# Optimization experiments

Hardware: AMD Instinct MI355X
Metric: run time of the kernel (lower is better)

The kernel has to match this reference:

```python
import jax, jax.numpy as jnp
import numpy as np

D = 8192          # dimension (high_dim_mode since > 1000)
M = 1_600_000     # ~0.05 * D*(D-1) pairs after the i>j mask
RIEMANN_SHIFT = 0.5


def _lower_tri_pairs(rng, d, m):
    # Sample m unique strictly-lower-triangular (i, j) positions (i > j).
    total = d * (d - 1) // 2
    k = rng.choice(total, size=m, replace=False)
    kf = k.astype(np.float64)
    i = np.floor((1.0 + np.sqrt(1.0 + 8.0 * kf)) / 2.0).astype(np.int64)
    # fix possible off-by-one from float sqrt
    tri = i * (i - 1) // 2
    i = np.where(tri > k, i - 1, i)
    tri = i * (i - 1) // 2
    j = k - tri
    return i, j


def setup_inputs() -> dict:
    key = jax.random.key(0)
    k1, k2 = jax.random.split(key)
    rng = np.random.default_rng(0)

    i, j = _lower_tri_pairs(rng, D, M)
    interaction_indices = jnp.asarray(np.stack([i, j]))  # [2, M] int64

    local_scale = 1.0 / D ** 0.75
    h_local = jax.random.normal(k1, (D,), dtype=jnp.float32) * local_scale + RIEMANN_SHIFT

    dim_factor = 1.0 / (D ** 0.9 * np.log(D))
    V_interaction = jax.random.normal(k2, (M,), dtype=jnp.float32) * dim_factor

    return {
        "h_local": h_local,
        "V_interaction": V_interaction,
        "interaction_indices": interaction_indices,
        "dimension": D,
    }


def reference(h_local, V_interaction, interaction_indices, dimension) -> jnp.ndarray:
    d = h_local.shape[0]
    # scatter interaction values into strict lower triangle (set semantics,
    # indices are unique so set == torch assignment)
    H_int = jnp.zeros((d, d), dtype=h_local.dtype)
    H_int = H_int.at[interaction_indices[0], interaction_indices[1]].set(V_interaction)
    H_int = H_int + H_int.T  # symmetrize
    interaction_scale = 1.0 - 0.2 / np.sqrt(np.log(dimension))
    return jnp.diag(h_local) + H_int * interaction_scale
```

## Files before the change

kernel.cpp:

```cpp
#include <hip/hip_runtime.h>
#include <math.h>


#define NCHUNK   512
#define NBKT     2048
#define BCAP     8
#define NROW     8192
#define OVB      512
#define OVCAP    64
#define SENTK    0xFFFFFFFFu
#define GCAP     65536


__global__ __launch_bounds__(1024) void p1_kernel(
    const int*   __restrict__ idx,
    const float* __restrict__ vals,
    float scale, int m, int cs,
    uint2* __restrict__ region1,
    uint2* __restrict__ ovfreg,
    int*   __restrict__ ovfcur,
    uint2* __restrict__ glist,
    int*   __restrict__ ghdr)
{
    __shared__ uint2 stage[NBKT][BCAP];
    __shared__ int   cnt[NBKT];
    __shared__ uint2 ovfst[OVB];
    __shared__ int   ovfn;
    uint2* sflat = &stage[0][0];
    const int tid = threadIdx.x;

    for (int c = 0; c < 2; ++c) {
        const int chunk = blockIdx.x * 2 + c;

        for (int f = tid; f < NBKT * BCAP; f += 1024) sflat[f] = make_uint2(SENTK, 0u);
        for (int b = tid; b < NBKT; b += 1024) cnt[b] = 0;
        if (tid == 0) ovfn = 0;
        __syncthreads();

        const int base = chunk * cs;
        int end = base + cs; if (end > m) end = m;
        for (int k = base + tid; k < end; k += 1024) {
            int i = idx[k];
            int j = idx[m + k];
            unsigned vb = __float_as_uint(vals[k] * scale);

            unsigned k1 = ((unsigned)i << 13) | (unsigned)j;
            int b1 = i >> 2;
            int p = atomicAdd(&cnt[b1], 1);
            if (p < BCAP) stage[b1][p] = make_uint2(k1, vb);
            else { int q = atomicAdd(&ovfn, 1);
                   if (q < OVB) ovfst[q] = make_uint2(k1, vb);
                   else { int g = atomicAdd(ghdr, 1); if (g < GCAP) glist[g] = make_uint2(k1, vb); } }

            unsigned k2 = ((unsigned)j << 13) | (unsigned)i;
            int b2 = j >> 2;
            p = atomicAdd(&cnt[b2], 1);
            if (p < BCAP) stage[b2][p] = make_uint2(k2, vb);
            else { int q = atomicAdd(&ovfn, 1);
                   if (q < OVB) ovfst[q] = make_uint2(k2, vb);
                   else { int g = atomicAdd(ghdr, 1); if (g < GCAP) glist[g] = make_uint2(k2, vb); } }
        }
        __syncthreads();

        for (int f = tid; f < NBKT * BCAP; f += 1024) {
            int bkt = f >> 3, e = f & 7;
            region1[((long long)bkt * NCHUNK + chunk) * BCAP + e] = sflat[f];
        }
        int n = ovfn; if (n > OVB) n = OVB;
        for (int e = tid; e < n; e += 1024) {
            uint2 en = ovfst[e];
            int row = en.x >> 13;
            int pos = atomicAdd(&ovfcur[row], 1);
            if (pos < OVCAP) ovfreg[row * OVCAP + pos] = en;
            else { int g = atomicAdd(ghdr, 1); if (g < GCAP) glist[g] = en; }
        }
        __syncthreads();
    }
}

__global__ __launch_bounds__(256) void rows9_kernel(
    float* __restrict__ out,
    const float* __restrict__ h_local,
    const uint2* __restrict__ region1,
    const uint2* __restrict__ ovfreg,
    const int*   __restrict__ ovfcur,
    const uint2* __restrict__ glist,
    const int*   __restrict__ ghdr)
{
    __shared__ float srow[8192];
    float4* s4 = reinterpret_cast<float4*>(srow);
    const int b   = blockIdx.x;
    const int row = ((b & 7) << 10) | (b >> 3);

    const float4 z = make_float4(0.f, 0.f, 0.f, 0.f);
    for (int c = threadIdx.x; c < 2048; c += 256) s4[c] = z;
    __syncthreads();

    const uint4* src = reinterpret_cast<const uint4*>(
        region1 + (long long)(row >> 2) * NCHUNK * BCAP);
    const unsigned ru = (unsigned)row;
    for (int e = threadIdx.x; e < (NCHUNK * BCAP) / 2; e += 256) {
        uint4 en = src[e];
        if ((en.x >> 13) == ru) srow[en.x & 8191] = __uint_as_float(en.y);
        if ((en.z >> 13) == ru) srow[en.z & 8191] = __uint_as_float(en.w);
    }
    int n = ovfcur[row]; if (n > OVCAP) n = OVCAP;
    for (int e = threadIdx.x; e < n; e += 256) {
        uint2 en = ovfreg[row * OVCAP + e];
        srow[en.x & 8191] = __uint_as_float(en.y);
    }
    int gn = ghdr[0];
    if (gn > 0) {
        if (gn > GCAP) gn = GCAP;
        for (int e = threadIdx.x; e < gn; e += 256) {
            uint2 en = glist[e];
            if ((en.x >> 13) == ru) srow[en.x & 8191] = __uint_as_float(en.y);
        }
    }
    if (threadIdx.x == 0) srow[row] = h_local[row];
    __syncthreads();

    float4* orow = reinterpret_cast<float4*>(out + ((long long)row << 13));
    for (int c = threadIdx.x; c < 2048; c += 256) orow[c] = s4[c];
}


__global__ __launch_bounds__(256) void init_counts_kernel(
    float* __restrict__ out, int d, int logd)
{
    int r = blockIdx.x * blockDim.x + threadIdx.x;
    if (r < d) reinterpret_cast<int*>(out)[(long long)r << logd] = 0;
}

__global__ __launch_bounds__(256) void bin_kernel(
    float* __restrict__ out,
    const int*   __restrict__ idx,
    const float* __restrict__ vals,
    float scale, int m, int logd, int cap)
{
    int k = blockIdx.x * blockDim.x + threadIdx.x;
    if (k >= m) return;
    int i = idx[k];
    int j = idx[m + k];
    unsigned vb = __float_as_uint(vals[k] * scale);
    int* cnt_i = reinterpret_cast<int*>(out) + ((long long)i << logd);
    int* cnt_j = reinterpret_cast<int*>(out) + ((long long)j << logd);
    int p1 = atomicAdd(cnt_i, 1);
    if (p1 < cap)
        *reinterpret_cast<uint2*>(out + ((long long)i << logd) + 2 + 2 * p1) =
            make_uint2((unsigned)j, vb);
    int p2 = atomicAdd(cnt_j, 1);
    if (p2 < cap)
        *reinterpret_cast<uint2*>(out + ((long long)j << logd) + 2 + 2 * p2) =
            make_uint2((unsigned)i, vb);
}

__global__ __launch_bounds__(256) void rows_kernel(
    float* __restrict__ out,
    const float* __restrict__ h_local,
    int logd, int cap)
{
    __shared__ float srow[8192];
    const int d  = 1 << logd;
    const int n4 = d >> 2;
    float4* s4 = reinterpret_cast<float4*>(srow);
    const int r = blockIdx.x;
    float* grow = out + ((long long)r << logd);
    const float4 z = make_float4(0.f, 0.f, 0.f, 0.f);
    for (int c = threadIdx.x; c < n4; c += blockDim.x) s4[c] = z;
    __syncthreads();
    int cnt = reinterpret_cast<const int*>(grow)[0];
    if (cnt > cap) cnt = cap;
    const uint2* eb = reinterpret_cast<const uint2*>(grow + 2);
    for (int e = threadIdx.x; e < cnt; e += blockDim.x) {
        uint2 p = eb[e];
        srow[p.x] = __uint_as_float(p.y);
    }
    if (threadIdx.x == 0) srow[r] = h_local[r];
    __syncthreads();
    for (int c = threadIdx.x; c < n4; c += blockDim.x)
        reinterpret_cast<float4*>(grow)[c] = s4[c];
}

__global__ __launch_bounds__(256) void fill_diag_kernel(
    float* __restrict__ out, const float* __restrict__ h_local,
    int d, long long n)
{
    long long t = (long long)blockIdx.x * blockDim.x + threadIdx.x;
    if (t >= n) return;
    long long row = t / d;
    long long col = t - row * d;
    out[t] = (row == col) ? h_local[row] : 0.f;
}

__global__ __launch_bounds__(256) void scatter_kernel(
    float* __restrict__ out,
    const int* __restrict__ idx,
    const float* __restrict__ vals,
    float scale, int m, int d)
{
    int k = blockIdx.x * blockDim.x + threadIdx.x;
    if (k >= m) return;
    int i = idx[k];
    int j = idx[m + k];
    float v = vals[k] * scale;
    out[(long long)i * d + j] = v;
    out[(long long)j * d + i] = v;
}


extern "C" void kernel_launch(void* const* d_in, const int* in_sizes, int n_in,
                              void* d_out, int out_size, void* d_ws, size_t ws_size,
                              hipStream_t stream) {
    const float* h_local = (const float*)d_in[0];
    const float* V_int   = (const float*)d_in[1];
    const int*   idx     = (const int*)d_in[2];

    const int d = in_sizes[0];
    const int m = in_sizes[1];

    int logd = 0;
    while ((1 << logd) < d) ++logd;
    const bool pow2 = ((1 << logd) == d);

    const float iscale = (float)(1.0 - 0.2 / sqrt(log((double)d)));
    float* out = (float*)d_out;
    const int block = 256;

    const size_t off_ovfcur = 4096;
    const size_t hdr_bytes  = off_ovfcur + (size_t)NROW * 4;
    const size_t off_glist  = 40960;
    const size_t off_ovfreg = off_glist + (size_t)GCAP * sizeof(uint2);
    const size_t off_r1     = off_ovfreg + (size_t)NROW * OVCAP * sizeof(uint2);
    const size_t ws_need    = off_r1 + (size_t)NBKT * NCHUNK * BCAP * sizeof(uint2);

    const bool path10 = (d == 8192) && (m > 0) && (m <= 2200000) &&
                        (d_ws != nullptr) && (ws_size >= ws_need);

    if (path10) {
        char* ws = (char*)d_ws;
        int*   ghdr    = (int*)ws;
        int*   ovfcur  = (int*)(ws + off_ovfcur);
        uint2* glist   = (uint2*)(ws + off_glist);
        uint2* ovfreg  = (uint2*)(ws + off_ovfreg);
        uint2* region1 = (uint2*)(ws + off_r1);

        const int cs = (m + NCHUNK - 1) / NCHUNK;

        hipMemsetAsync(ws, 0, hdr_bytes, stream);
        p1_kernel<<<NCHUNK / 2, 1024, 0, stream>>>(idx, V_int, iscale, m, cs,
                                                   region1, ovfreg, ovfcur,
                                                   glist, ghdr);
        rows9_kernel<<<NROW, 256, 0, stream>>>(out, h_local, region1,
                                               ovfreg, ovfcur, glist, ghdr);
    } else if (pow2 && d >= 1024 && d <= 8192 &&
               ((long long)m * 2 / d) < (long long)((d - 2) / 2) / 2) {
        const int cap = (d - 2) / 2;
        init_counts_kernel<<<(d + block - 1) / block, block, 0, stream>>>(out, d, logd);
        bin_kernel<<<(m + block - 1) / block, block, 0, stream>>>(out, idx, V_int,
                                                                  iscale, m, logd, cap);
        rows_kernel<<<d, block, 0, stream>>>(out, h_local, logd, cap);
    } else {
        const long long n = (long long)d * d;
        const long long grid_fill = (n + block - 1) / block;
        fill_diag_kernel<<<(dim3)(unsigned)grid_fill, block, 0, stream>>>(out, h_local, d, n);
        const int grid_sc = (m + block - 1) / block;
        scatter_kernel<<<grid_sc, block, 0, stream>>>(out, idx, V_int, iscale, m, d);
    }
}
```

Before: 357.3 us.

## Pack bucketed entries contiguously per 4-row bucket via global atomic offsets

Replaces the fixed per-chunk sentinel-padded bucket slots with a compacted per-bucket list. Each producer block reserves space in a global per-bucket cursor and writes only its real entries. The row kernel now handles four rows per block and scans only the packed bucket entries instead of every padded chunk slot. This cuts the padding traffic both in the write and in the read phase. In exchange it adds global atomics per bucket per block, and each block scans its bucket list four times.

```diff
diff --git a/kernel.cpp b/kernel.cpp
--- a/kernel.cpp
+++ b/kernel.cpp
@@ -2,44 +2,35 @@
 #include <math.h>
 
 
-#define NCHUNK   512
+#define P1_PAIRS 4096
 #define NBKT     2048
 #define BCAP     8
-#define NROW     8192
-#define OVB      512
-#define OVCAP    64
-#define SENTK    0xFFFFFFFFu
+#define PCAP     2048
 #define GCAP     65536
 
 
 __global__ __launch_bounds__(1024) void p1_kernel(
     const int*   __restrict__ idx,
     const float* __restrict__ vals,
-    float scale, int m, int cs,
-    uint2* __restrict__ region1,
-    uint2* __restrict__ ovfreg,
-    int*   __restrict__ ovfcur,
+    float scale, int m,
+    uint2* __restrict__ packed,
+    int*   __restrict__ gcur,
     uint2* __restrict__ glist,
     int*   __restrict__ ghdr)
 {
     __shared__ uint2 stage[NBKT][BCAP];
     __shared__ int   cnt[NBKT];
-    __shared__ uint2 ovfst[OVB];
-    __shared__ int   ovfn;
-    uint2* sflat = &stage[0][0];
+    __shared__ int   off[NBKT];
     const int tid = threadIdx.x;
 
-    for (int c = 0; c < 2; ++c) {
-        const int chunk = blockIdx.x * 2 + c;
-
-        for (int f = tid; f < NBKT * BCAP; f += 1024) sflat[f] = make_uint2(SENTK, 0u);
-        for (int b = tid; b < NBKT; b += 1024) cnt[b] = 0;
-        if (tid == 0) ovfn = 0;
-        __syncthreads();
-
-        const int base = chunk * cs;
-        int end = base + cs; if (end > m) end = m;
-        for (int k = base + tid; k < end; k += 1024) {
+    for (int b = tid; b < NBKT; b += 1024) cnt[b] = 0;
+    __syncthreads();
+
+    const int base = blockIdx.x * P1_PAIRS;
+#pragma unroll
+    for (int it = 0; it < P1_PAIRS / 1024; ++it) {
+        int k = base + it * 1024 + tid;
+        if (k < m) {
             int i = idx[k];
             int j = idx[m + k];
             unsigned vb = __float_as_uint(vals[k] * scale);
@@ -48,80 +39,80 @@
             int b1 = i >> 2;
             int p = atomicAdd(&cnt[b1], 1);
             if (p < BCAP) stage[b1][p] = make_uint2(k1, vb);
-            else { int q = atomicAdd(&ovfn, 1);
-                   if (q < OVB) ovfst[q] = make_uint2(k1, vb);
-                   else { int g = atomicAdd(ghdr, 1); if (g < GCAP) glist[g] = make_uint2(k1, vb); } }
+            else { int g = atomicAdd(&gcur[b1], 1);
+                   if (g < PCAP) packed[(long long)b1 * PCAP + g] = make_uint2(k1, vb);
+                   else { int q = atomicAdd(ghdr, 1); if (q < GCAP) glist[q] = make_uint2(k1, vb); } }
 
             unsigned k2 = ((unsigned)j << 13) | (unsigned)i;
             int b2 = j >> 2;
             p = atomicAdd(&cnt[b2], 1);
             if (p < BCAP) stage[b2][p] = make_uint2(k2, vb);
-            else { int q = atomicAdd(&ovfn, 1);
-                   if (q < OVB) ovfst[q] = make_uint2(k2, vb);
-                   else { int g = atomicAdd(ghdr, 1); if (g < GCAP) glist[g] = make_uint2(k2, vb); } }
-        }
-        __syncthreads();
-
-        for (int f = tid; f < NBKT * BCAP; f += 1024) {
-            int bkt = f >> 3, e = f & 7;
-            region1[((long long)bkt * NCHUNK + chunk) * BCAP + e] = sflat[f];
-        }
-        int n = ovfn; if (n > OVB) n = OVB;
-        for (int e = tid; e < n; e += 1024) {
-            uint2 en = ovfst[e];
-            int row = en.x >> 13;
-            int pos = atomicAdd(&ovfcur[row], 1);
-            if (pos < OVCAP) ovfreg[row * OVCAP + pos] = en;
-            else { int g = atomicAdd(ghdr, 1); if (g < GCAP) glist[g] = en; }
-        }
-        __syncthreads();
-    }
-}
-
-__global__ __launch_bounds__(256) void rows9_kernel(
+            else { int g = atomicAdd(&gcur[b2], 1);
+                   if (g < PCAP) packed[(long long)b2 * PCAP + g] = make_uint2(k2, vb);
+                   else { int q = atomicAdd(ghdr, 1); if (q < GCAP) glist[q] = make_uint2(k2, vb); } }
+        }
+    }
+    __syncthreads();
+
+    for (int b = tid; b < NBKT; b += 1024) {
+        int c = cnt[b]; if (c > BCAP) c = BCAP;
+        off[b] = (c > 0) ? atomicAdd(&gcur[b], c) : 0;
+    }
+    __syncthreads();
+
+    for (int f = tid; f < NBKT * BCAP; f += 1024) {
+        int b = f >> 3, e = f & 7;
+        int c = cnt[b]; if (c > BCAP) c = BCAP;
+        if (e < c) {
+            int pos = off[b] + e;
+            if (pos < PCAP) packed[(long long)b * PCAP + pos] = stage[b][e];
+            else { int q = atomicAdd(ghdr, 1); if (q < GCAP) glist[q] = stage[b][e]; }
+        }
+    }
+}
+
+__global__ __launch_bounds__(256) void p2_kernel(
     float* __restrict__ out,
     const float* __restrict__ h_local,
-    const uint2* __restrict__ region1,
-    const uint2* __restrict__ ovfreg,
-    const int*   __restrict__ ovfcur,
+    const uint2* __restrict__ packed,
+    const int*   __restrict__ gcur,
     const uint2* __restrict__ glist,
     const int*   __restrict__ ghdr)
 {
     __shared__ float srow[8192];
     float4* s4 = reinterpret_cast<float4*>(srow);
     const int b   = blockIdx.x;
-    const int row = ((b & 7) << 10) | (b >> 3);
+    const int tid = threadIdx.x;
+
+    int n = gcur[b]; if (n > PCAP) n = PCAP;
+    int gn = ghdr[0]; if (gn > GCAP) gn = GCAP;
+    const uint2* pb = packed + (long long)b * PCAP;
 
     const float4 z = make_float4(0.f, 0.f, 0.f, 0.f);
-    for (int c = threadIdx.x; c < 2048; c += 256) s4[c] = z;
-    __syncthreads();
-
-    const uint4* src = reinterpret_cast<const uint4*>(
-        region1 + (long long)(row >> 2) * NCHUNK * BCAP);
-    const unsigned ru = (unsigned)row;
-    for (int e = threadIdx.x; e < (NCHUNK * BCAP) / 2; e += 256) {
-        uint4 en = src[e];
-        if ((en.x >> 13) == ru) srow[en.x & 8191] = __uint_as_float(en.y);
-        if ((en.z >> 13) == ru) srow[en.z & 8191] = __uint_as_float(en.w);
-    }
-    int n = ovfcur[row]; if (n > OVCAP) n = OVCAP;
-    for (int e = threadIdx.x; e < n; e += 256) {
-        uint2 en = ovfreg[row * OVCAP + e];
-        srow[en.x & 8191] = __uint_as_float(en.y);
-    }
-    int gn = ghdr[0];
-    if (gn > 0) {
-        if (gn > GCAP) gn = GCAP;
-        for (int e = threadIdx.x; e < gn; e += 256) {
-            uint2 en = glist[e];
+    for (int r4 = 0; r4 < 4; ++r4) {
+        const int row = (b << 2) + r4;
+        const unsigned ru = (unsigned)row;
+
+        for (int c = tid; c < 2048; c += 256) s4[c] = z;
+        __syncthreads();
+
+        for (int e = tid; e < n; e += 256) {
+            uint2 en = pb[e];
             if ((en.x >> 13) == ru) srow[en.x & 8191] = __uint_as_float(en.y);
         }
-    }
-    if (threadIdx.x == 0) srow[row] = h_local[row];
-    __syncthreads();
-
-    float4* orow = reinterpret_cast<float4*>(out + ((long long)row << 13));
-    for (int c = threadIdx.x; c < 2048; c += 256) orow[c] = s4[c];
+        if (gn > 0) {
+            for (int e = tid; e < gn; e += 256) {
+                uint2 en = glist[e];
+                if ((en.x >> 13) == ru) srow[en.x & 8191] = __uint_as_float(en.y);
+            }
+        }
+        if (tid == 0) srow[row] = h_local[row];
+        __syncthreads();
+
+        float4* orow = reinterpret_cast<float4*>(out + ((long long)row << 13));
+        for (int c = tid; c < 2048; c += 256) orow[c] = s4[c];
+        __syncthreads();
+    }
 }
 
 
@@ -227,32 +218,29 @@
     float* out = (float*)d_out;
     const int block = 256;
 
-    const size_t off_ovfcur = 4096;
-    const size_t hdr_bytes  = off_ovfcur + (size_t)NROW * 4;
-    const size_t off_glist  = 40960;
-    const size_t off_ovfreg = off_glist + (size_t)GCAP * sizeof(uint2);
-    const size_t off_r1     = off_ovfreg + (size_t)NROW * OVCAP * sizeof(uint2);
-    const size_t ws_need    = off_r1 + (size_t)NBKT * NCHUNK * BCAP * sizeof(uint2);
-
-    const bool path10 = (d == 8192) && (m > 0) && (m <= 2200000) &&
+    const size_t off_ghdr   = 8192;
+    const size_t hdr_bytes  = 12288;
+    const size_t off_glist  = 12288;
+    const size_t off_packed = off_glist + (size_t)GCAP * sizeof(uint2);
+    const size_t ws_need    = off_packed + (size_t)NBKT * PCAP * sizeof(uint2);
+
+    const bool path12 = (d == 8192) && (m > 0) && (m <= 1700000) &&
                         (d_ws != nullptr) && (ws_size >= ws_need);
 
-    if (path10) {
+    if (path12) {
         char* ws = (char*)d_ws;
-        int*   ghdr    = (int*)ws;
-        int*   ovfcur  = (int*)(ws + off_ovfcur);
-        uint2* glist   = (uint2*)(ws + off_glist);
-        uint2* ovfreg  = (uint2*)(ws + off_ovfreg);
-        uint2* region1 = (uint2*)(ws + off_r1);
-
-        const int cs = (m + NCHUNK - 1) / NCHUNK;
+        int*   gcur   = (int*)ws;
+        int*   ghdr   = (int*)(ws + off_ghdr);
+        uint2* glist  = (uint2*)(ws + off_glist);
+        uint2* packed = (uint2*)(ws + off_packed);
+
+        const int nblk = (m + P1_PAIRS - 1) / P1_PAIRS;
 
         hipMemsetAsync(ws, 0, hdr_bytes, stream);
-        p1_kernel<<<NCHUNK / 2, 1024, 0, stream>>>(idx, V_int, iscale, m, cs,
-                                                   region1, ovfreg, ovfcur,
-                                                   glist, ghdr);
-        rows9_kernel<<<NROW, 256, 0, stream>>>(out, h_local, region1,
-                                               ovfreg, ovfcur, glist, ghdr);
+        p1_kernel<<<nblk, 1024, 0, stream>>>(idx, V_int, iscale, m,
+                                             packed, gcur, glist, ghdr);
+        p2_kernel<<<NBKT, 256, 0, stream>>>(out, h_local, packed, gcur,
+                                            glist, ghdr);
     } else if (pow2 && d >= 1024 && d <= 8192 &&
                ((long long)m * 2 / d) < (long long)((d - 2) / 2) / 2) {
         const int cap = (d - 2) / 2;
```

Result: faster. 328.8 us (-8.0%).
